# Kernel optimization log

Measured on AMD Instinct MI355X. Metric: run time of the kernel, lower is better.

Reference implementation:

```python
import jax, jax.numpy as jnp
import numpy as np
import math

B, S, D, H = 2, 2048, 1024, 16
HD = D // H


def setup_inputs() -> dict:
    key = jax.random.key(0)
    ks = jax.random.split(key, 8)
    sc = 0.02
    return {
        "x": jax.random.normal(ks[0], (B, S, D), dtype=jnp.float32),
        "y": jax.random.normal(ks[1], (B, S, D), dtype=jnp.float32),
        "W_kv": jax.random.normal(ks[2], (D, 2 * D), dtype=jnp.float32) * sc,
        "b_kv": jnp.zeros((2 * D,), dtype=jnp.float32),
        "W_q": jax.random.normal(ks[3], (D, D), dtype=jnp.float32) * sc,
        "b_q": jnp.zeros((D,), dtype=jnp.float32),
        "W_o": jax.random.normal(ks[4], (D, D), dtype=jnp.float32) * sc,
        "b_o": jnp.zeros((D,), dtype=jnp.float32),
    }


def reference(x, y, W_kv, b_kv, W_q, b_q, W_o, b_o):
    b, s, d = x.shape
    h, hd = H, HD
    # kv projection from x (the "context"), q projection from y
    kv = x @ W_kv + b_kv                     # [b, s, 2d]
    q = y @ W_q + b_q                        # [b, s, d]
    kv = kv.reshape(b, s, h, 2 * hd).transpose(0, 2, 1, 3)  # [b, h, s, 2hd]
    q = q.reshape(b, s, h, hd).transpose(0, 2, 1, 3)        # [b, h, s, hd]
    k, v = kv[..., :hd], kv[..., hd:]
    scaled = jnp.einsum("bhqd,bhkd->bhqk", q, k) / math.sqrt(hd)  # [b,h,s,s]
    attention = jax.nn.softmax(scaled, axis=-1)  # F.softmax defaults to last dim
    values = jnp.einsum("bhqk,bhkd->bhqd", attention, v)  # [b, h, s, hd]
    # Faithful to the original: reshape [b,h,s,hd] -> [b,s,d] WITHOUT
    # transposing heads back (row-major flatten, heads interleaved).
    values = values.reshape(b, s, d)
    return values @ W_o + b_o
```

## Files before the change

### kernel.cpp

```cpp
#include <hip/hip_runtime.h>
#include <hip/hip_bf16.h>


#define S_LEN 2048
#define D_DIM 1024
#define H_NUM 16
#define HD_DIM 64

typedef __attribute__((ext_vector_type(8))) __bf16 bf16x8;
typedef __attribute__((ext_vector_type(4))) float f32x4;

__device__ __forceinline__ unsigned short f2bf(float f) {
    unsigned int v;
    __builtin_memcpy(&v, &f, 4);
    v = v + 0x7fff + ((v >> 16) & 1);
    return (unsigned short)(v >> 16);
}
__device__ __forceinline__ unsigned int pkbf(float a, float b) {
    __hip_bfloat162 h = __float22bfloat162_rn(float2{a, b});
    unsigned int r;
    __builtin_memcpy(&r, &h, 4);
    return r;
}
__device__ __forceinline__ float sani(float v) {
    unsigned int u;
    __builtin_memcpy(&u, &v, 4);
    return ((u >> 23) & 0xFFu) == 0xFFu ? 0.f : v;
}
__device__ __forceinline__ void gll16(const void* g, void* l) {
    __builtin_amdgcn_global_load_lds(
        (const __attribute__((address_space(1))) void*)g,
        (__attribute__((address_space(3))) void*)l, 16, 0, 0);
}

__global__ __launch_bounds__(256) void prep(const float* __restrict__ Wkv,
                                            const float* __restrict__ Wq,
                                            const float* __restrict__ Wo,
                                            const float* __restrict__ x,
                                            unsigned short* __restrict__ WkvT,
                                            unsigned short* __restrict__ WqT,
                                            unsigned short* __restrict__ WoT,
                                            unsigned short* __restrict__ xbf) {
    __shared__ unsigned short tile[32][33];
    const int blk = blockIdx.x;
    if (blk < 4096) {
        const float* in; unsigned short* out; int C, bx, by;
        if (blk < 2048)      { in = Wkv; out = WkvT; C = 2048; bx = blk & 63;          by = blk >> 6; }
        else if (blk < 3072) { in = Wq;  out = WqT;  C = 1024; bx = (blk - 2048) & 31; by = (blk - 2048) >> 5; }
        else                 { in = Wo;  out = WoT;  C = 1024; bx = (blk - 3072) & 31; by = (blk - 3072) >> 5; }
        const int R = 1024;
        int c0 = bx * 32, r0 = by * 32;
        int tx = threadIdx.x & 31, ty = threadIdx.x >> 5;
        for (int i = 0; i < 32; i += 8)
            tile[ty + i][tx] = f2bf(in[(size_t)(r0 + ty + i) * C + c0 + tx]);
        __syncthreads();
        for (int i = 0; i < 32; i += 8)
            out[(size_t)(c0 + ty + i) * R + r0 + tx] = tile[tx][ty + i];
    } else {
        int i = ((blk - 4096) * 256 + threadIdx.x) * 8;
        float4 a0 = *(const float4*)&x[i];
        float4 a1 = *(const float4*)&x[i + 4];
        uint4 p;
        p.x = pkbf(a0.x, a0.y); p.y = pkbf(a0.z, a0.w);
        p.z = pkbf(a1.x, a1.y); p.w = pkbf(a1.z, a1.w);
        *(uint4*)&xbf[i] = p;
    }
}

__global__ __launch_bounds__(256) void proj(const unsigned short* __restrict__ xbf,
                                            const float* __restrict__ y,
                                            const unsigned short* __restrict__ WkvT,
                                            const unsigned short* __restrict__ WqT,
                                            const float* __restrict__ b_kv,
                                            const float* __restrict__ b_q,
                                            unsigned short* __restrict__ Kb,
                                            unsigned short* __restrict__ VtB,
                                            unsigned short* __restrict__ qBuf,
                                            int base) {
    __shared__ unsigned short sA[2][128 * 32];
    __shared__ unsigned short sB[2][128 * 32];

    const int cpx = gridDim.x >> 3;
    const int swz = (blockIdx.x & 7) * cpx + (blockIdx.x >> 3);
    const int blk = swz + base;

    const bool iskv = blk < 512;
    const int bid = iskv ? blk : blk - 512;
    const int m0 = iskv ? (bid >> 4) * 128 : (bid >> 3) * 128;
    const int n0 = iskv ? (bid & 15) * 128 : (bid & 7) * 128;
    const unsigned short* Bt = iskv ? WkvT : WqT;
    const int tid = threadIdx.x;
    const int w = tid >> 6, lane = tid & 63;
    const int quad = lane >> 4, lm = lane & 15;
    const int wrow = (w >> 1) * 64, wcol = (w & 1) * 64;

    const int srow = tid >> 2;
    const int scol = (tid & 3) << 3;

    auto stageB = [&](int k0, int bsel) {
#pragma unroll
        for (int p = 0; p < 2; ++p) {
            int cid = p * 256 + tid;
            gll16(&Bt[(size_t)(n0 + srow + p * 64) * 1024 + k0 + scol], &sB[bsel][cid * 8]);
        }
    };
    auto stageAkv = [&](int k0, int bsel) {
#pragma unroll
        for (int p = 0; p < 2; ++p) {
            int cid = p * 256 + tid;
            gll16(&xbf[(size_t)(m0 + srow + p * 64) * 1024 + k0 + scol], &sA[bsel][cid * 8]);
        }
    };

    f32x4 acc[4][4] = {};

    if (iskv) {
        stageAkv(0, 0);
    } else {
        const float* Af = y + (size_t)(m0 + srow) * 1024 + scol;
        float4 a0 = *(const float4*)Af;
        float4 a1 = *(const float4*)(Af + 4);
        float4 a2 = *(const float4*)(Af + 65536);
        float4 a3 = *(const float4*)(Af + 65536 + 4);
        uint4 pk;
        pk.x = pkbf(a0.x, a0.y); pk.y = pkbf(a0.z, a0.w);
        pk.z = pkbf(a1.x, a1.y); pk.w = pkbf(a1.z, a1.w);
        *(uint4*)&sA[0][tid * 8] = pk;
        pk.x = pkbf(a2.x, a2.y); pk.y = pkbf(a2.z, a2.w);
        pk.z = pkbf(a3.x, a3.y); pk.w = pkbf(a3.z, a3.w);
        *(uint4*)&sA[0][(256 + tid) * 8] = pk;
    }
    stageB(0, 0);
    __syncthreads();

    int cur = 0;
    for (int t = 0; t < 32; ++t) {
        const int nb = cur ^ 1;
        const int nk0 = (t + 1) * 32;
        float4 a0, a1, a2, a3;
        if (t < 31) {
            if (iskv) {
                stageAkv(nk0, nb);
            } else {
                const float* Af = y + (size_t)(m0 + srow) * 1024 + nk0 + scol;
                a0 = *(const float4*)Af;
                a1 = *(const float4*)(Af + 4);
                a2 = *(const float4*)(Af + 65536);
                a3 = *(const float4*)(Af + 65536 + 4);
            }
            stageB(nk0, nb);
        }

        bf16x8 av[4], bv[4];
#pragma unroll
        for (int i = 0; i < 4; ++i)
            av[i] = *(const bf16x8*)&sA[cur][(wrow + i * 16 + lm) * 32 + quad * 8];
#pragma unroll
        for (int j = 0; j < 4; ++j)
            bv[j] = *(const bf16x8*)&sB[cur][(wcol + j * 16 + lm) * 32 + quad * 8];
#pragma unroll
        for (int i = 0; i < 4; ++i)
#pragma unroll
            for (int j = 0; j < 4; ++j)
                acc[i][j] = __builtin_amdgcn_mfma_f32_16x16x32_bf16(av[i], bv[j], acc[i][j], 0, 0, 0);

        if (t < 31 && !iskv) {
            uint4 pk;
            pk.x = pkbf(a0.x, a0.y); pk.y = pkbf(a0.z, a0.w);
            pk.z = pkbf(a1.x, a1.y); pk.w = pkbf(a1.z, a1.w);
            *(uint4*)&sA[nb][tid * 8] = pk;
            pk.x = pkbf(a2.x, a2.y); pk.y = pkbf(a2.z, a2.w);
            pk.z = pkbf(a3.x, a3.y); pk.w = pkbf(a3.z, a3.w);
            *(uint4*)&sA[nb][(256 + tid) * 8] = pk;
        }
        __syncthreads();
        cur = nb;
    }

    if (iskv) {
        const int h = n0 >> 7;
        if (wcol == 0) {
#pragma unroll
            for (int i = 0; i < 4; ++i)
#pragma unroll
                for (int j = 0; j < 4; ++j) {
                    int d = j * 16 + lm;
                    float bi = b_kv[h * 128 + d];
#pragma unroll
                    for (int r = 0; r < 4; ++r) {
                        int grow = m0 + wrow + i * 16 + quad * 4 + r;
                        int bb = grow >> 11, ss = grow & 2047;
                        Kb[((size_t)(bb * 16 + h) * 2048 + ss) * 64 + d] =
                            f2bf(sani(acc[i][j][r] + bi));
                    }
                }
        } else {
#pragma unroll
            for (int i = 0; i < 4; ++i)
#pragma unroll
                for (int j = 0; j < 4; ++j) {
                    int d = j * 16 + lm;
                    float bi = b_kv[h * 128 + 64 + d];
                    int s0 = m0 + wrow + i * 16 + quad * 4;
                    int bb = s0 >> 11, ss = s0 & 2047;
                    ushort4 u;
                    u.x = f2bf(sani(acc[i][j][0] + bi));
                    u.y = f2bf(sani(acc[i][j][1] + bi));
                    u.z = f2bf(sani(acc[i][j][2] + bi));
                    u.w = f2bf(sani(acc[i][j][3] + bi));
                    *(ushort4*)&VtB[((size_t)(bb * 16 + h) * 64 + d) * 2048 + ss] = u;
                }
        }
    } else {
#pragma unroll
        for (int i = 0; i < 4; ++i)
#pragma unroll
            for (int j = 0; j < 4; ++j)
#pragma unroll
                for (int r = 0; r < 4; ++r) {
                    int grow = m0 + wrow + i * 16 + quad * 4 + r;
                    int gcol = n0 + wcol + j * 16 + lm;
                    float val = sani(acc[i][j][r] + b_q[gcol]) * 0.1803368801f;
                    qBuf[(size_t)grow * 1024 + gcol] = f2bf(val);
                }
    }
}

__global__ __launch_bounds__(256) void attn_k(unsigned short* qo,
                                              const unsigned short* __restrict__ Kb,
                                              const unsigned short* __restrict__ Vt) {
    __shared__ unsigned short sK[2][2][64 * 32];
    __shared__ unsigned short sVt[2][2][64 * 32];
    __shared__ unsigned short sP[4][16 * 64];

    const int tid = threadIdx.x;
    const int w = tid >> 6, lane = tid & 63;
    const int quad = lane >> 4, lm = lane & 15;

    const int cpx = gridDim.x >> 3;
    const int swz = (blockIdx.x & 7) * cpx + (blockIdx.x >> 3);
    const int qblock = swz & 31;
    const int bh = swz >> 5;
    const int b = bh >> 4, h = bh & 15;

    unsigned short* Qp = qo + (size_t)b * S_LEN * D_DIM + h * HD_DIM;
    const unsigned short* Kbase = Kb + (size_t)bh * S_LEN * HD_DIM;
    const unsigned short* Vbase = Vt + (size_t)bh * HD_DIM * S_LEN;

    const int qrow0 = qblock * 64 + w * 16;
    bf16x8 qa0 = *(const bf16x8*)&Qp[(size_t)(qrow0 + lm) * D_DIM + quad * 8];
    bf16x8 qa1 = *(const bf16x8*)&Qp[(size_t)(qrow0 + lm) * D_DIM + 32 + quad * 8];

    f32x4 acc_o[4] = {};
    float lsum[4] = {0.f, 0.f, 0.f, 0.f};

    const int srow = tid >> 2;
    const int sch = (tid & 3) << 3;

    unsigned short* sPw = sP[w];
    int sprow[4], spgx[4];
#pragma unroll
    for (int r = 0; r < 4; ++r) {
        int row = quad * 4 + r;
        sprow[r] = row * 64 + (lm ^ ((row & 1) << 3));
        spgx[r] = (row >> 1) & 3;
    }
    const unsigned short* pa0p = &sPw[(lm * 64 + quad * 8) ^ ((lm & 7) << 3)];
    const unsigned short* pa1p = &sPw[(lm * 64 + 32 + quad * 8) ^ ((lm & 7) << 3)];

    auto stage = [&](int kt, int bsel) {
        const unsigned short* Kr = Kbase + (size_t)(kt * 64 + srow) * 64 + sch;
        gll16(Kr,      &sK[bsel][0][tid * 8]);
        gll16(Kr + 32, &sK[bsel][1][tid * 8]);
        const unsigned short* Vr = Vbase + (size_t)srow * 2048 + kt * 64 + sch;
        gll16(Vr,      &sVt[bsel][0][tid * 8]);
        gll16(Vr + 32, &sVt[bsel][1][tid * 8]);
    };

    stage(0, 0);
    __syncthreads();

    int cur = 0;
    for (int kt = 0; kt < S_LEN / 64; ++kt) {
        const int nb = cur ^ 1;
        if (kt < S_LEN / 64 - 1) stage(kt + 1, nb);

#pragma unroll
        for (int g = 0; g < 4; ++g) {
            bf16x8 k0 = *(const bf16x8*)&sK[cur][0][(g * 16 + lm) * 32 + quad * 8];
            bf16x8 k1 = *(const bf16x8*)&sK[cur][1][(g * 16 + lm) * 32 + quad * 8];
            f32x4 z = {0.f, 0.f, 0.f, 0.f};
            __builtin_amdgcn_s_setprio(1);
            f32x4 c = __builtin_amdgcn_mfma_f32_16x16x32_bf16(
                          qa1, k1,
                          __builtin_amdgcn_mfma_f32_16x16x32_bf16(qa0, k0, z, 0, 0, 0),
                          0, 0, 0);
            __builtin_amdgcn_s_setprio(0);
            float p0 = __builtin_amdgcn_exp2f(c[0]);
            float p1 = __builtin_amdgcn_exp2f(c[1]);
            float p2 = __builtin_amdgcn_exp2f(c[2]);
            float p3 = __builtin_amdgcn_exp2f(c[3]);
            lsum[0] += p0; lsum[1] += p1; lsum[2] += p2; lsum[3] += p3;
            unsigned int v01 = pkbf(p0, p1);
            unsigned int v23 = pkbf(p2, p3);
            sPw[sprow[0] + ((g ^ spgx[0]) << 4)] = (unsigned short)v01;
            sPw[sprow[1] + ((g ^ spgx[1]) << 4)] = (unsigned short)(v01 >> 16);
            sPw[sprow[2] + ((g ^ spgx[2]) << 4)] = (unsigned short)v23;
            sPw[sprow[3] + ((g ^ spgx[3]) << 4)] = (unsigned short)(v23 >> 16);
        }
        bf16x8 pa0 = *(const bf16x8*)pa0p;
        bf16x8 pa1 = *(const bf16x8*)pa1p;
#pragma unroll
        for (int n = 0; n < 4; ++n) {
            bf16x8 v0 = *(const bf16x8*)&sVt[cur][0][(n * 16 + lm) * 32 + quad * 8];
            bf16x8 v1 = *(const bf16x8*)&sVt[cur][1][(n * 16 + lm) * 32 + quad * 8];
            __builtin_amdgcn_s_setprio(1);
            acc_o[n] = __builtin_amdgcn_mfma_f32_16x16x32_bf16(
                           pa1, v1,
                           __builtin_amdgcn_mfma_f32_16x16x32_bf16(pa0, v0, acc_o[n], 0, 0, 0),
                           0, 0, 0);
            __builtin_amdgcn_s_setprio(0);
        }
        __syncthreads();
        cur = nb;
    }

#pragma unroll
    for (int r = 0; r < 4; ++r) {
#pragma unroll
        for (int off = 1; off < 16; off <<= 1)
            lsum[r] += __shfl_xor(lsum[r], off);
        float inv = 1.f / lsum[r];
        int qrow = qrow0 + quad * 4 + r;
#pragma unroll
        for (int n = 0; n < 4; ++n)
            Qp[(size_t)qrow * D_DIM + n * 16 + lm] = f2bf(sani(acc_o[n][r] * inv));
    }
}

__global__ __launch_bounds__(256) void fgemm(const unsigned short* __restrict__ O,
                                             const unsigned short* __restrict__ WoT,
                                             const float* __restrict__ b_o,
                                             float* __restrict__ out) {
    __shared__ unsigned short sA[2][64 * 32];
    __shared__ unsigned short sB[2][128 * 32];
    const int tid = threadIdx.x;
    const int m0 = blockIdx.y * 64;
    const int n0 = blockIdx.x * 128;
    const int w = tid >> 6, lane = tid & 63;
    const int quad = lane >> 4, lm = lane & 15;
    const int wrow = (w >> 1) * 32, wcol = (w & 1) * 64;

    auto stage = [&](int k0, int bsel) {
        {
            int row = tid >> 2, kk = k0 + ((tid & 3) << 3);
            int m = m0 + row;
            int bb = m >> 11, sib = m & 2047;
            int hh = sib >> 7, qhi = sib & 127;
            gll16(&O[(size_t)((bb << 11) + (qhi << 4) + (kk >> 6)) * 1024 + (hh << 6) + (kk & 63)],
                  &sA[bsel][tid * 8]);
        }
#pragma unroll
        for (int p = 0; p < 2; ++p) {
            int cid = p * 256 + tid;
            int row = cid >> 2, col = (cid & 3) << 3;
            gll16(&WoT[(size_t)(n0 + row) * 1024 + k0 + col], &sB[bsel][cid * 8]);
        }
    };

    f32x4 acc[2][4] = {};

    stage(0, 0);
    __syncthreads();

    int cur = 0;
    for (int t = 0; t < 32; ++t) {
        const int nb = cur ^ 1;
        if (t < 31) stage((t + 1) * 32, nb);

        bf16x8 av[2], bv[4];
#pragma unroll
        for (int i = 0; i < 2; ++i)
            av[i] = *(const bf16x8*)&sA[cur][(wrow + i * 16 + lm) * 32 + quad * 8];
#pragma unroll
        for (int j = 0; j < 4; ++j)
            bv[j] = *(const bf16x8*)&sB[cur][(wcol + j * 16 + lm) * 32 + quad * 8];
#pragma unroll
        for (int i = 0; i < 2; ++i)
#pragma unroll
            for (int j = 0; j < 4; ++j)
                acc[i][j] = __builtin_amdgcn_mfma_f32_16x16x32_bf16(av[i], bv[j], acc[i][j], 0, 0, 0);

        __syncthreads();
        cur = nb;
    }

#pragma unroll
    for (int i = 0; i < 2; ++i)
#pragma unroll
        for (int j = 0; j < 4; ++j)
#pragma unroll
            for (int r = 0; r < 4; ++r) {
                int grow = m0 + wrow + i * 16 + quad * 4 + r;
                int gcol = n0 + wcol + j * 16 + lm;
                out[(size_t)grow * 1024 + gcol] = sani(acc[i][j][r] + b_o[gcol]);
            }
}

__global__ __launch_bounds__(256) void fill_k(float* out, int n) {
    int i = blockIdx.x * 256 + threadIdx.x;
    if (i < n) out[i] = 4.0f;
}

extern "C" void kernel_launch(void* const* d_in, const int* in_sizes, int n_in,
                              void* d_out, int out_size, void* d_ws, size_t ws_size,
                              hipStream_t stream) {
    const float* x    = (const float*)d_in[0];
    const float* y    = (const float*)d_in[1];
    const float* W_kv = (const float*)d_in[2];
    const float* b_kv = (const float*)d_in[3];
    const float* W_q  = (const float*)d_in[4];
    const float* b_q  = (const float*)d_in[5];
    const float* W_o  = (const float*)d_in[6];
    const float* b_o  = (const float*)d_in[7];

    if (ws_size < (size_t)16 * 1024 * 1024) {
        fill_k<<<dim3((out_size + 255) / 256), 256, 0, stream>>>((float*)d_out, out_size);
        return;
    }
    const bool bigws = ws_size >= (size_t)26 * 1024 * 1024;

    unsigned short* ws   = (unsigned short*)d_ws;
    unsigned short* Kb   = ws;
    unsigned short* VtB  = ws + 4 * 1024 * 1024;
    unsigned short* xbf  = (unsigned short*)d_out;
    unsigned short* WkvT = xbf + 4 * 1024 * 1024;
    unsigned short* WqT  = WkvT + 2 * 1024 * 1024;
    unsigned short* WoT  = bigws ? ws + 12 * 1024 * 1024
                                 : WqT + 1024 * 1024;
    unsigned short* qBuf = bigws ? ws + 8 * 1024 * 1024
                                 : xbf;
    float* outBuf        = bigws ? (float*)d_out : (float*)d_ws;

    prep<<<dim3(6144), 256, 0, stream>>>(W_kv, W_q, W_o, x, WkvT, WqT, WoT, xbf);
    if (bigws) {
        proj<<<dim3(768), 256, 0, stream>>>(xbf, y, WkvT, WqT, b_kv, b_q, Kb, VtB, qBuf, 0);
    } else {
        proj<<<dim3(512), 256, 0, stream>>>(xbf, y, WkvT, WqT, b_kv, b_q, Kb, VtB, qBuf, 0);
        proj<<<dim3(256), 256, 0, stream>>>(xbf, y, WkvT, WqT, b_kv, b_q, Kb, VtB, qBuf, 512);
    }
    attn_k<<<dim3(2 * H_NUM * (S_LEN / 64)), 256, 0, stream>>>(qBuf, Kb, VtB);
    fgemm<<<dim3(8, 64), 256, 0, stream>>>(qBuf, WoT, b_o, outBuf);
    if (!bigws)
        hipMemcpyAsync(d_out, d_ws, (size_t)out_size * sizeof(float),
                       hipMemcpyDeviceToDevice, stream);
}
```

Measured before the change: 240.9 us.

## Software-pipeline attention loop: overlap PV of previous tile with QK of current

Restructures the attention inner loop so the P·V MFMAs for tile kt-1 run after the QK^T and exp work of tile kt, with V fragments and P fragments preloaded into registers at the end of each iteration. This is meant to hide LDS latency and the exp/pack dependency chain behind independent matrix work. It also adds a launch-bounds occupancy hint of 4 blocks per CU. The extra live register arrays raise register pressure, which under the occupancy cap could cause spills.

```diff
diff --git a/kernel.cpp b/kernel.cpp
--- a/kernel.cpp
+++ b/kernel.cpp
@@ -226,9 +226,9 @@
     }
 }
 
-__global__ __launch_bounds__(256) void attn_k(unsigned short* qo,
-                                              const unsigned short* __restrict__ Kb,
-                                              const unsigned short* __restrict__ Vt) {
+__global__ __launch_bounds__(256, 4) void attn_k(unsigned short* qo,
+                                                 const unsigned short* __restrict__ Kb,
+                                                 const unsigned short* __restrict__ Vt) {
     __shared__ unsigned short sK[2][2][64 * 32];
     __shared__ unsigned short sVt[2][2][64 * 32];
     __shared__ unsigned short sP[4][16 * 64];
@@ -253,6 +253,9 @@
 
     f32x4 acc_o[4] = {};
     float lsum[4] = {0.f, 0.f, 0.f, 0.f};
+
+    bf16x8 vr0[4], vr1[4];
+    bf16x8 pa0, pa1;
 
     const int srow = tid >> 2;
     const int sch = (tid & 3) << 3;
@@ -277,18 +280,11 @@
         gll16(Vr + 32, &sVt[bsel][1][tid * 8]);
     };
 
-    stage(0, 0);
-    __syncthreads();
-
-    int cur = 0;
-    for (int kt = 0; kt < S_LEN / 64; ++kt) {
-        const int nb = cur ^ 1;
-        if (kt < S_LEN / 64 - 1) stage(kt + 1, nb);
-
+    auto qk = [&](const unsigned short* sKc) {
 #pragma unroll
         for (int g = 0; g < 4; ++g) {
-            bf16x8 k0 = *(const bf16x8*)&sK[cur][0][(g * 16 + lm) * 32 + quad * 8];
-            bf16x8 k1 = *(const bf16x8*)&sK[cur][1][(g * 16 + lm) * 32 + quad * 8];
+            bf16x8 k0 = *(const bf16x8*)&sKc[(g * 16 + lm) * 32 + quad * 8];
+            bf16x8 k1 = *(const bf16x8*)&sKc[64 * 32 + (g * 16 + lm) * 32 + quad * 8];
             f32x4 z = {0.f, 0.f, 0.f, 0.f};
             __builtin_amdgcn_s_setprio(1);
             f32x4 c = __builtin_amdgcn_mfma_f32_16x16x32_bf16(
@@ -308,22 +304,51 @@
             sPw[sprow[2] + ((g ^ spgx[2]) << 4)] = (unsigned short)v23;
             sPw[sprow[3] + ((g ^ spgx[3]) << 4)] = (unsigned short)(v23 >> 16);
         }
-        bf16x8 pa0 = *(const bf16x8*)pa0p;
-        bf16x8 pa1 = *(const bf16x8*)pa1p;
+    };
+
+    auto pv = [&]() {
+        __builtin_amdgcn_s_setprio(1);
+#pragma unroll
+        for (int n = 0; n < 4; ++n)
+            acc_o[n] = __builtin_amdgcn_mfma_f32_16x16x32_bf16(
+                           pa1, vr1[n],
+                           __builtin_amdgcn_mfma_f32_16x16x32_bf16(pa0, vr0[n], acc_o[n], 0, 0, 0),
+                           0, 0, 0);
+        __builtin_amdgcn_s_setprio(0);
+    };
+
+    auto vload = [&](const unsigned short* sVc) {
 #pragma unroll
         for (int n = 0; n < 4; ++n) {
-            bf16x8 v0 = *(const bf16x8*)&sVt[cur][0][(n * 16 + lm) * 32 + quad * 8];
-            bf16x8 v1 = *(const bf16x8*)&sVt[cur][1][(n * 16 + lm) * 32 + quad * 8];
-            __builtin_amdgcn_s_setprio(1);
-            acc_o[n] = __builtin_amdgcn_mfma_f32_16x16x32_bf16(
-                           pa1, v1,
-                           __builtin_amdgcn_mfma_f32_16x16x32_bf16(pa0, v0, acc_o[n], 0, 0, 0),
-                           0, 0, 0);
-            __builtin_amdgcn_s_setprio(0);
-        }
+            vr0[n] = *(const bf16x8*)&sVc[(n * 16 + lm) * 32 + quad * 8];
+            vr1[n] = *(const bf16x8*)&sVc[64 * 32 + (n * 16 + lm) * 32 + quad * 8];
+        }
+    };
+    auto paload = [&]() {
+        pa0 = *(const bf16x8*)pa0p;
+        pa1 = *(const bf16x8*)pa1p;
+    };
+
+    stage(0, 0);
+    __syncthreads();
+
+    stage(1, 1);
+    qk(&sK[0][0][0]);
+    vload(&sVt[0][0][0]);
+    paload();
+    __syncthreads();
+
+    int cur = 1;
+    for (int kt = 1; kt < 32; ++kt) {
+        if (kt < 31) stage(kt + 1, cur ^ 1);
+        qk(&sK[cur][0][0]);
+        pv();
+        vload(&sVt[cur][0][0]);
+        paload();
         __syncthreads();
-        cur = nb;
-    }
+        cur ^= 1;
+    }
+    pv();
 
 #pragma unroll
     for (int r = 0; r < 4; ++r) {
```

Measured after the change: 246.4 us. 1.02x slower.

## Load K/V directly into registers and process two query tiles per wave

Applied to the files above, without the earlier changes.

The attention kernel stops staging K and V tiles through shared memory with block barriers. Instead each wave loads its K and V fragments straight from global memory into registers and software-pipelines the next tile's loads behind compute. Each wave now handles 32 query rows (two 16-row tiles) so every register-loaded K/V fragment is reused twice, and the grid halves to 512 blocks with a launch bound of 2. This removes the __syncthreads and the LDS traffic for K/V, at the cost of redundant global/L2 reads across the four waves of a block, higher register pressure, and fewer blocks for the GPU's CUs.

```diff
diff --git a/kernel.cpp b/kernel.cpp
--- a/kernel.cpp
+++ b/kernel.cpp
@@ -226,12 +226,10 @@
     }
 }
 
-__global__ __launch_bounds__(256) void attn_k(unsigned short* qo,
-                                              const unsigned short* __restrict__ Kb,
-                                              const unsigned short* __restrict__ Vt) {
-    __shared__ unsigned short sK[2][2][64 * 32];
-    __shared__ unsigned short sVt[2][2][64 * 32];
-    __shared__ unsigned short sP[4][16 * 64];
+__global__ __launch_bounds__(256, 2) void attn_k(unsigned short* qo,
+                                                 const unsigned short* __restrict__ Kb,
+                                                 const unsigned short* __restrict__ Vt) {
+    __shared__ unsigned short sP[4][2][16 * 64];
 
     const int tid = threadIdx.x;
     const int w = tid >> 6, lane = tid & 63;
@@ -239,25 +237,30 @@
 
     const int cpx = gridDim.x >> 3;
     const int swz = (blockIdx.x & 7) * cpx + (blockIdx.x >> 3);
-    const int qblock = swz & 31;
-    const int bh = swz >> 5;
+    const int qblock = swz & 15;
+    const int bh = swz >> 4;
     const int b = bh >> 4, h = bh & 15;
 
     unsigned short* Qp = qo + (size_t)b * S_LEN * D_DIM + h * HD_DIM;
     const unsigned short* Kbase = Kb + (size_t)bh * S_LEN * HD_DIM;
     const unsigned short* Vbase = Vt + (size_t)bh * HD_DIM * S_LEN;
 
-    const int qrow0 = qblock * 64 + w * 16;
-    bf16x8 qa0 = *(const bf16x8*)&Qp[(size_t)(qrow0 + lm) * D_DIM + quad * 8];
-    bf16x8 qa1 = *(const bf16x8*)&Qp[(size_t)(qrow0 + lm) * D_DIM + 32 + quad * 8];
-
-    f32x4 acc_o[4] = {};
-    float lsum[4] = {0.f, 0.f, 0.f, 0.f};
-
-    const int srow = tid >> 2;
-    const int sch = (tid & 3) << 3;
-
-    unsigned short* sPw = sP[w];
+    const int qrow0 = qblock * 128 + w * 32;
+
+    bf16x8 qa[2][2];
+#pragma unroll
+    for (int qb = 0; qb < 2; ++qb) {
+        qa[qb][0] = *(const bf16x8*)&Qp[(size_t)(qrow0 + qb * 16 + lm) * D_DIM + quad * 8];
+        qa[qb][1] = *(const bf16x8*)&Qp[(size_t)(qrow0 + qb * 16 + lm) * D_DIM + 32 + quad * 8];
+    }
+
+    f32x4 acc_o[2][4] = {};
+    float lsum[2][4] = {};
+
+    bf16x8 kr[2][4];
+    bf16x8 vr[2][4];
+    bf16x8 pa[2][2];
+
     int sprow[4], spgx[4];
 #pragma unroll
     for (int r = 0; r < 4; ++r) {
@@ -265,42 +268,43 @@
         sprow[r] = row * 64 + (lm ^ ((row & 1) << 3));
         spgx[r] = (row >> 1) & 3;
     }
-    const unsigned short* pa0p = &sPw[(lm * 64 + quad * 8) ^ ((lm & 7) << 3)];
-    const unsigned short* pa1p = &sPw[(lm * 64 + 32 + quad * 8) ^ ((lm & 7) << 3)];
-
-    auto stage = [&](int kt, int bsel) {
-        const unsigned short* Kr = Kbase + (size_t)(kt * 64 + srow) * 64 + sch;
-        gll16(Kr,      &sK[bsel][0][tid * 8]);
-        gll16(Kr + 32, &sK[bsel][1][tid * 8]);
-        const unsigned short* Vr = Vbase + (size_t)srow * 2048 + kt * 64 + sch;
-        gll16(Vr,      &sVt[bsel][0][tid * 8]);
-        gll16(Vr + 32, &sVt[bsel][1][tid * 8]);
-    };
-
-    stage(0, 0);
-    __syncthreads();
-
-    int cur = 0;
-    for (int kt = 0; kt < S_LEN / 64; ++kt) {
-        const int nb = cur ^ 1;
-        if (kt < S_LEN / 64 - 1) stage(kt + 1, nb);
-
+    unsigned short* sP0 = sP[w][0];
+    unsigned short* sP1 = sP[w][1];
+    const int rd0 = (lm * 64 + quad * 8) ^ ((lm & 7) << 3);
+    const int rd1 = (lm * 64 + 32 + quad * 8) ^ ((lm & 7) << 3);
+
+    auto loadK = [&](int kt) {
 #pragma unroll
         for (int g = 0; g < 4; ++g) {
-            bf16x8 k0 = *(const bf16x8*)&sK[cur][0][(g * 16 + lm) * 32 + quad * 8];
-            bf16x8 k1 = *(const bf16x8*)&sK[cur][1][(g * 16 + lm) * 32 + quad * 8];
+            const unsigned short* p = Kbase + (size_t)(kt * 64 + g * 16 + lm) * 64 + quad * 8;
+            kr[0][g] = *(const bf16x8*)p;
+            kr[1][g] = *(const bf16x8*)(p + 32);
+        }
+    };
+    auto loadV = [&](int kt) {
+#pragma unroll
+        for (int n = 0; n < 4; ++n) {
+            const unsigned short* p = Vbase + (size_t)(n * 16 + lm) * 2048 + kt * 64 + quad * 8;
+            vr[0][n] = *(const bf16x8*)p;
+            vr[1][n] = *(const bf16x8*)(p + 32);
+        }
+    };
+
+    auto qk = [&](int qb, unsigned short* sPw) {
+#pragma unroll
+        for (int g = 0; g < 4; ++g) {
             f32x4 z = {0.f, 0.f, 0.f, 0.f};
             __builtin_amdgcn_s_setprio(1);
             f32x4 c = __builtin_amdgcn_mfma_f32_16x16x32_bf16(
-                          qa1, k1,
-                          __builtin_amdgcn_mfma_f32_16x16x32_bf16(qa0, k0, z, 0, 0, 0),
+                          qa[qb][1], kr[1][g],
+                          __builtin_amdgcn_mfma_f32_16x16x32_bf16(qa[qb][0], kr[0][g], z, 0, 0, 0),
                           0, 0, 0);
             __builtin_amdgcn_s_setprio(0);
             float p0 = __builtin_amdgcn_exp2f(c[0]);
             float p1 = __builtin_amdgcn_exp2f(c[1]);
             float p2 = __builtin_amdgcn_exp2f(c[2]);
             float p3 = __builtin_amdgcn_exp2f(c[3]);
-            lsum[0] += p0; lsum[1] += p1; lsum[2] += p2; lsum[3] += p3;
+            lsum[qb][0] += p0; lsum[qb][1] += p1; lsum[qb][2] += p2; lsum[qb][3] += p3;
             unsigned int v01 = pkbf(p0, p1);
             unsigned int v23 = pkbf(p2, p3);
             sPw[sprow[0] + ((g ^ spgx[0]) << 4)] = (unsigned short)v01;
@@ -308,34 +312,60 @@
             sPw[sprow[2] + ((g ^ spgx[2]) << 4)] = (unsigned short)v23;
             sPw[sprow[3] + ((g ^ spgx[3]) << 4)] = (unsigned short)(v23 >> 16);
         }
-        bf16x8 pa0 = *(const bf16x8*)pa0p;
-        bf16x8 pa1 = *(const bf16x8*)pa1p;
-#pragma unroll
-        for (int n = 0; n < 4; ++n) {
-            bf16x8 v0 = *(const bf16x8*)&sVt[cur][0][(n * 16 + lm) * 32 + quad * 8];
-            bf16x8 v1 = *(const bf16x8*)&sVt[cur][1][(n * 16 + lm) * 32 + quad * 8];
-            __builtin_amdgcn_s_setprio(1);
-            acc_o[n] = __builtin_amdgcn_mfma_f32_16x16x32_bf16(
-                           pa1, v1,
-                           __builtin_amdgcn_mfma_f32_16x16x32_bf16(pa0, v0, acc_o[n], 0, 0, 0),
-                           0, 0, 0);
-            __builtin_amdgcn_s_setprio(0);
-        }
-        __syncthreads();
-        cur = nb;
-    }
-
-#pragma unroll
-    for (int r = 0; r < 4; ++r) {
-#pragma unroll
-        for (int off = 1; off < 16; off <<= 1)
-            lsum[r] += __shfl_xor(lsum[r], off);
-        float inv = 1.f / lsum[r];
-        int qrow = qrow0 + quad * 4 + r;
+    };
+
+    auto pv = [&](int qb) {
+        __builtin_amdgcn_s_setprio(1);
 #pragma unroll
         for (int n = 0; n < 4; ++n)
-            Qp[(size_t)qrow * D_DIM + n * 16 + lm] = f2bf(sani(acc_o[n][r] * inv));
-    }
+            acc_o[qb][n] = __builtin_amdgcn_mfma_f32_16x16x32_bf16(
+                               pa[qb][1], vr[1][n],
+                               __builtin_amdgcn_mfma_f32_16x16x32_bf16(pa[qb][0], vr[0][n],
+                                                                       acc_o[qb][n], 0, 0, 0),
+                               0, 0, 0);
+        __builtin_amdgcn_s_setprio(0);
+    };
+
+    auto paload = [&]() {
+        pa[0][0] = *(const bf16x8*)&sP0[rd0];
+        pa[0][1] = *(const bf16x8*)&sP0[rd1];
+        pa[1][0] = *(const bf16x8*)&sP1[rd0];
+        pa[1][1] = *(const bf16x8*)&sP1[rd1];
+    };
+
+    loadK(0);
+    loadV(0);
+    qk(0, sP0);
+    qk(1, sP1);
+    loadK(1);
+    paload();
+
+    for (int kt = 1; kt < 32; ++kt) {
+        pv(0);
+        pv(1);
+        loadV(kt);
+        qk(0, sP0);
+        qk(1, sP1);
+        if (kt < 31) loadK(kt + 1);
+        paload();
+    }
+    pv(0);
+    pv(1);
+
+#pragma unroll
+    for (int qb = 0; qb < 2; ++qb)
+#pragma unroll
+        for (int r = 0; r < 4; ++r) {
+            float s = lsum[qb][r];
+#pragma unroll
+            for (int off = 1; off < 16; off <<= 1)
+                s += __shfl_xor(s, off);
+            float inv = 1.f / s;
+            int qrow = qrow0 + qb * 16 + quad * 4 + r;
+#pragma unroll
+            for (int n = 0; n < 4; ++n)
+                Qp[(size_t)qrow * D_DIM + n * 16 + lm] = f2bf(sani(acc_o[qb][n][r] * inv));
+        }
 }
 
 __global__ __launch_bounds__(256) void fgemm(const unsigned short* __restrict__ O,
@@ -449,7 +479,7 @@
         proj<<<dim3(512), 256, 0, stream>>>(xbf, y, WkvT, WqT, b_kv, b_q, Kb, VtB, qBuf, 0);
         proj<<<dim3(256), 256, 0, stream>>>(xbf, y, WkvT, WqT, b_kv, b_q, Kb, VtB, qBuf, 512);
     }
-    attn_k<<<dim3(2 * H_NUM * (S_LEN / 64)), 256, 0, stream>>>(qBuf, Kb, VtB);
+    attn_k<<<dim3(512), 256, 0, stream>>>(qBuf, Kb, VtB);
     fgemm<<<dim3(8, 64), 256, 0, stream>>>(qBuf, WoT, b_o, outBuf);
     if (!bigws)
         hipMemcpyAsync(d_out, d_ws, (size_t)out_size * sizeof(float),
```

After: 291.7 us. +21.1%, slower.
